# Kernel optimization log

Measured on AMD Instinct MI355X. Metric: run time of the kernel, lower is better.

The kernel has to match this reference:

```python
import jax, jax.numpy as jnp
import numpy as np

N, D, H, O = 2048, 128, 256, 1  # batch, input_dim, hidden_dim, output_dim
LN_EPS = 1e-5


def setup_inputs() -> dict:
    key = jax.random.key(0)
    ks = jax.random.split(key, 10)
    s = lambda fan_in: 1.0 / np.sqrt(fan_in)
    return {
        "array": jax.random.normal(ks[0], (N, D), dtype=jnp.float32),
        # per-feature Linear(1, H) stacked: weight [D, H], bias [D, H]
        "W_in": jax.random.uniform(ks[1], (D, H), jnp.float32, -1.0, 1.0),
        "b_in": jax.random.uniform(ks[2], (D, H), jnp.float32, -1.0, 1.0),
        # FactorAttentionLayer (width D): W: Linear(D, D), V: Linear(D, 1), LayerNorm(D)
        "Wf": jax.random.uniform(ks[3], (D, D), jnp.float32, -s(D), s(D)),
        "bf": jax.random.uniform(ks[4], (D,), jnp.float32, -s(D), s(D)),
        "Vf": jax.random.uniform(ks[5], (D,), jnp.float32, -s(D), s(D)),
        "bv": jnp.zeros((), jnp.float32),
        "ln_g": jnp.ones((D,), jnp.float32),
        "ln_b": jnp.zeros((D,), jnp.float32),
        # fc_hidden: Linear(D*H, H); fc_output: Linear(H, O)  (stored as [in, out])
        "Wh": jax.random.uniform(ks[6], (D * H, H), jnp.float32, -s(D * H), s(D * H)),
        "bh": jax.random.uniform(ks[7], (H,), jnp.float32, -s(D * H), s(D * H)),
        "Wo": jax.random.uniform(ks[8], (H, O), jnp.float32, -s(H), s(H)),
        "bo": jax.random.uniform(ks[9], (O,), jnp.float32, -s(H), s(H)),
    }


def reference(array, W_in, b_in, Wf, bf, Vf, bv, ln_g, ln_b, Wh, bh, Wo, bo):
    # Fused per-feature Linear(1,H)+ReLU: [n, D, H]
    p = jax.nn.relu(array[:, :, None] * W_in[None] + b_in[None])
    # permute(0, 2, 1) -> [n, H, D]
    x = jnp.transpose(p, (0, 2, 1))
    # FactorAttention: tanh-linear, softmax over axis 1 (the H axis), residual mul, LayerNorm over D
    u = jnp.tanh(jnp.einsum('nhd,de->nhe', x, Wf) + bf)          # [n, H, D]
    scores = jnp.einsum('nhd,d->nh', u, Vf) + bv                  # [n, H]
    attn = jax.nn.softmax(scores, axis=1)[:, :, None]             # [n, H, 1]
    y = x + x * attn                                              # [n, H, D]
    mu = jnp.mean(y, axis=-1, keepdims=True)
    var = jnp.mean((y - mu) ** 2, axis=-1, keepdims=True)
    y = (y - mu) * jax.lax.rsqrt(var + LN_EPS) * ln_g + ln_b
    # flatten [n, H*D] and MLP head (dropout = identity in eval)
    xx = y.reshape(y.shape[0], -1)
    h = jax.nn.relu(xx @ Wh + bh)
    return h @ Wo + bo
```

## Files before the change

kernel.cpp:

```cpp
#include <hip/hip_runtime.h>

#define NB 2048
#define DD 128
#define HH 256
#define KF 32768
#define LN_EPS 1e-5f
#define KSPLIT 32
#define KSL (KF / KSPLIT)

typedef __attribute__((ext_vector_type(8))) short short8;
typedef __attribute__((ext_vector_type(4))) float float4_t;
typedef __attribute__((ext_vector_type(4))) float f4;

__device__ __forceinline__ unsigned short f2bf(float f) {
    unsigned int u = __builtin_bit_cast(unsigned int, f);
    u += 0x7fffu + ((u >> 16) & 1u);
    return (unsigned short)(u >> 16);
}

__device__ __forceinline__ unsigned int pkbf(float lo, float hi) {
    unsigned int r;
    asm("v_cvt_pk_bf16_f32 %0, %1, %2" : "=v"(r) : "v"(lo), "v"(hi));
    return r;
}

__device__ __forceinline__ void gl2lds16(const void* g, void* l) {
    __builtin_amdgcn_global_load_lds(
        (const __attribute__((address_space(1))) unsigned int*)g,
        (__attribute__((address_space(3))) unsigned int*)l, 16, 0, 0);
}

__global__ void prep_all(const float* __restrict__ arr, const float* __restrict__ Win,
                         const float* __restrict__ bin, const float* __restrict__ Wh,
                         const float* __restrict__ g, const float* __restrict__ beta,
                         float2* __restrict__ stats, float* __restrict__ WinT,
                         float* __restrict__ binT, unsigned short* __restrict__ WhbT,
                         float* __restrict__ bias2) {
    __shared__ float a_s[4][128];
    __shared__ float tile32[32][33];
    __shared__ unsigned short tile64[64][65];
    __shared__ float red[4][64];
    int bid = blockIdx.x;
    int t = threadIdx.x;

    if (bid >= 576) {
        int pid = bid - 576;
        int kb = pid >> 2;
        int jb = pid & 3;
        int c = t & 63, r4 = t >> 6;
        int k0 = kb * 64;
        float bsum = 0.f;
        for (int rr = r4; rr < 64; rr += 4) {
            int k = k0 + rr, d = k & 127;
            float v = Wh[(long)k * 256 + jb * 64 + c];
            tile64[rr][c] = f2bf(g[d] * v);
            bsum = fmaf(beta[d], v, bsum);
        }
        __syncthreads();
        for (int rr = r4; rr < 64; rr += 4)
            WhbT[(long)(jb * 64 + rr) * KF + k0 + c] = tile64[c][rr];
        red[r4][c] = bsum;
        __syncthreads();
        if (r4 == 0)
            atomicAdd(&bias2[jb * 64 + c],
                      red[0][c] + red[1][c] + red[2][c] + red[3][c]);
        return;
    }
    if (bid >= 512) {
        int tid = bid - 512;
        int mat = tid >> 5;
        int dt = (tid >> 3) & 3;
        int ht = tid & 7;
        const float* src = mat ? bin : Win;
        float* dst = mat ? binT : WinT;
        int c = t & 31, r = t >> 5;
#pragma unroll
        for (int rr = r; rr < 32; rr += 8)
            tile32[rr][c] = src[(dt * 32 + rr) * 256 + ht * 32 + c];
        __syncthreads();
#pragma unroll
        for (int rr = r; rr < 32; rr += 8)
            dst[(ht * 32 + rr) * 128 + dt * 32 + c] = tile32[c][rr];
        return;
    }
    int n0 = bid * 4;
    for (int i = t; i < 512; i += 256) a_s[i >> 7][i & 127] = arr[n0 * 128 + i];
    __syncthreads();
    int h = t;
    float sum[4] = {0.f, 0.f, 0.f, 0.f}, ssq[4] = {0.f, 0.f, 0.f, 0.f};
    for (int d = 0; d < 128; ++d) {
        float w = Win[d * 256 + h];
        float bb = bin[d * 256 + h];
#pragma unroll
        for (int q = 0; q < 4; ++q) {
            float x = fmaxf(fmaf(a_s[q][d], w, bb), 0.f);
            sum[q] += x;
            ssq[q] = fmaf(x, x, ssq[q]);
        }
    }
#pragma unroll
    for (int q = 0; q < 4; ++q) {
        float mu = sum[q] * (1.f / 128.f);
        float var = fmaxf(ssq[q] * (1.f / 128.f) - mu * mu, 0.f);
        float rs = rsqrtf(var + LN_EPS);
        stats[(long)(n0 + q) * HH + h] = make_float2(rs, mu * rs);
    }
}

__global__ __launch_bounds__(512, 4) void gemm_f(
        const float* __restrict__ arr, const float* __restrict__ WinT,
        const float* __restrict__ binT, const float2* __restrict__ stats,
        const unsigned short* __restrict__ Bt,
        float* __restrict__ Cp) {
    __shared__ unsigned short Bs[2][256 * 32];
    __shared__ float Ws[8 * 128];
    __shared__ float Vs[8 * 128];
    __shared__ float2 Ss[128 * 9];
    int bid = blockIdx.x;
    int xcd = bid & 7;
    int idx = bid >> 3;
    int ks = xcd * 4 + (idx >> 4);
    int mt = idx & 15;
    int m0 = mt * 128;
    long k0 = (long)ks * KSL;
    int h0 = ks * 8;
    int t = threadIdx.x;
    int lane = t & 63, wave = t >> 6;
    int wm = (wave >> 1) * 32;
    int wn = (wave & 1) * 128;
    int fr = lane & 15;
    int kch = lane >> 4;
    int fk8 = kch * 8;

    float4_t acc[2][8] = {};

    const unsigned short* Bab = Bt + k0;
    int j0 = t >> 2, sl0 = t & 3;
    long boff0 = (long)j0 * KF + (long)((sl0 ^ ((j0 >> 1) & 3)) << 3);
    long boff1 = boff0 + 128l * KF;

    if (t < 256) {
        *(f4*)&Ws[t * 4] = *(const f4*)(WinT + h0 * 128 + t * 4);
    } else {
        *(f4*)&Vs[(t - 256) * 4] = *(const f4*)(binT + h0 * 128 + (t - 256) * 4);
    }
    {
        int sr = t >> 2, sc = (t & 3) * 2;
        const float2* sp = stats + (long)(m0 + sr) * HH + h0 + sc;
        float2 v0 = sp[0], v1 = sp[1];
        Ss[sr * 9 + sc] = v0;
        Ss[sr * 9 + sc + 1] = v1;
    }
    gl2lds16(Bab + boff0, &Bs[0][t * 8]);
    gl2lds16(Bab + boff1, &Bs[0][(t + 512) * 8]);

    int row0 = m0 + wm + fr;
    f4 aa[2][2];
    __syncthreads();

    for (int it = 0; it < 32; ++it) {
        int q = it >> 3, hl = it & 7, cur = it & 1;
        if (it < 31) {
            int itn = it + 1;
            long kap = (itn & 7) * 128 + (itn >> 3) * 32;
            gl2lds16(Bab + kap + boff0, &Bs[cur ^ 1][t * 8]);
            gl2lds16(Bab + kap + boff1, &Bs[cur ^ 1][(t + 512) * 8]);
        }
        if (hl == 0) {
#pragma unroll
            for (int mi = 0; mi < 2; ++mi) {
                const float* ap = arr + (long)(row0 + mi * 16) * DD + q * 32 + fk8;
                aa[mi][0] = *(const f4*)ap;
                aa[mi][1] = *(const f4*)(ap + 4);
            }
        }
        int wb = hl * 128 + q * 32 + fk8;
        f4 w0 = *(const f4*)&Ws[wb], w1 = *(const f4*)&Ws[wb + 4];
        f4 v0 = *(const f4*)&Vs[wb], v1 = *(const f4*)&Vs[wb + 4];
        short8 af[2];
#pragma unroll
        for (int mi = 0; mi < 2; ++mi) {
            float2 sv = Ss[(wm + mi * 16 + fr) * 9 + hl];
            float rs = sv.x, nm = -sv.y;
            float z0 = fmaf(fmaxf(fmaf(aa[mi][0][0], w0[0], v0[0]), 0.f), rs, nm);
            float z1 = fmaf(fmaxf(fmaf(aa[mi][0][1], w0[1], v0[1]), 0.f), rs, nm);
            float z2 = fmaf(fmaxf(fmaf(aa[mi][0][2], w0[2], v0[2]), 0.f), rs, nm);
            float z3 = fmaf(fmaxf(fmaf(aa[mi][0][3], w0[3], v0[3]), 0.f), rs, nm);
            float z4 = fmaf(fmaxf(fmaf(aa[mi][1][0], w1[0], v1[0]), 0.f), rs, nm);
            float z5 = fmaf(fmaxf(fmaf(aa[mi][1][1], w1[1], v1[1]), 0.f), rs, nm);
            float z6 = fmaf(fmaxf(fmaf(aa[mi][1][2], w1[2], v1[2]), 0.f), rs, nm);
            float z7 = fmaf(fmaxf(fmaf(aa[mi][1][3], w1[3], v1[3]), 0.f), rs, nm);
            union { short8 s; unsigned int u[4]; } pk;
            pk.u[0] = pkbf(z0, z1);
            pk.u[1] = pkbf(z2, z3);
            pk.u[2] = pkbf(z4, z5);
            pk.u[3] = pkbf(z6, z7);
            af[mi] = pk.s;
        }
#pragma unroll
        for (int half = 0; half < 2; ++half) {
            short8 bfv[4];
#pragma unroll
            for (int n4 = 0; n4 < 4; ++n4) {
                int j = wn + (half * 4 + n4) * 16 + fr;
                bfv[n4] = *(const short8*)&Bs[cur][j * 32 + ((kch ^ ((j >> 1) & 3)) << 3)];
            }
#pragma unroll
            for (int mi = 0; mi < 2; ++mi)
#pragma unroll
                for (int n4 = 0; n4 < 4; ++n4)
                    acc[mi][half * 4 + n4] = __builtin_amdgcn_mfma_f32_16x16x32_bf16(
                        af[mi], bfv[n4], acc[mi][half * 4 + n4], 0, 0, 0);
        }
        if (it < 31) __syncthreads();
    }

    int rb = (lane >> 4) * 4;
    float* Cb = Cp + (long)ks * NB * 256;
#pragma unroll
    for (int mi = 0; mi < 2; ++mi) {
#pragma unroll
        for (int ni = 0; ni < 8; ++ni) {
            int n = wn + ni * 16 + fr;
#pragma unroll
            for (int r = 0; r < 4; ++r) {
                int m = m0 + wm + mi * 16 + rb + r;
                Cb[(long)m * 256 + n] = acc[mi][ni][r];
            }
        }
    }
}

__global__ void finale(const float* __restrict__ Cp, const float* __restrict__ bh,
                       const float* __restrict__ Wo, const float* __restrict__ bo,
                       const float* __restrict__ bias2, float* __restrict__ out) {
    __shared__ float red[4];
    int n = blockIdx.x, t = threadIdx.x;
    int lane = t & 63, wave = t >> 6;
    float s = bh[t] + bias2[t];
    for (int sl = 0; sl < KSPLIT; ++sl)
        s += Cp[(long)sl * NB * 256 + (long)n * 256 + t];
    float v = fmaxf(s, 0.f) * Wo[t];
#pragma unroll
    for (int o = 32; o; o >>= 1) v += __shfl_down(v, o);
    if (lane == 0) red[wave] = v;
    __syncthreads();
    if (t == 0) out[n] = red[0] + red[1] + red[2] + red[3] + bo[0];
}

extern "C" void kernel_launch(void* const* d_in, const int* in_sizes, int n_in,
                              void* d_out, int out_size, void* d_ws, size_t ws_size,
                              hipStream_t stream) {
    const float* arr  = (const float*)d_in[0];
    const float* Win  = (const float*)d_in[1];
    const float* bin  = (const float*)d_in[2];
    const float* ln_g = (const float*)d_in[7];
    const float* ln_b = (const float*)d_in[8];
    const float* Wh   = (const float*)d_in[9];
    const float* bh   = (const float*)d_in[10];
    const float* Wo   = (const float*)d_in[11];
    const float* bo   = (const float*)d_in[12];
    float* out = (float*)d_out;

    char* ws = (char*)d_ws;
    unsigned short* WhbT = (unsigned short*)ws;
    float2* stats = (float2*)(ws + 16777216ull);
    float* Cp     = (float*)(ws + 20971520ull);
    float* WinT   = (float*)(ws + 88080384ull);
    float* binT   = (float*)(ws + 88211456ull);
    float* bias2  = (float*)(ws + 88342528ull);

    hipMemsetAsync(bias2, 0, 1024, stream);
    hipLaunchKernelGGL(prep_all, dim3(2624), dim3(256), 0, stream,
                       arr, Win, bin, Wh, ln_g, ln_b, stats, WinT, binT, WhbT, bias2);
    hipLaunchKernelGGL(gemm_f, dim3(512), dim3(512), 0, stream,
                       arr, WinT, binT, stats, WhbT, Cp);
    hipLaunchKernelGGL(finale, dim3(NB), dim3(256), 0, stream,
                       Cp, bh, Wo, bo, bias2, out);
}
```

Measured before the change: 179.6 us.

## Triple-buffer B tiles with prefetch distance two and drop bias atomics

The GEMM's LDS staging for B goes from double to triple buffering. Loads are issued two iterations ahead and guarded by explicit vmcnt waits and raw barriers instead of __syncthreads, so global-to-LDS latency is hidden better. The bias atomicAdd and its memset are replaced by per-block partial sums, which the first four GEMM blocks reduce before starting their main work. The cost is more LDS per block, which may cut occupancy, plus some extra serial work in four blocks.

```diff
diff --git a/kernel.cpp b/kernel.cpp
--- a/kernel.cpp
+++ b/kernel.cpp
@@ -35,7 +35,7 @@
                          const float* __restrict__ g, const float* __restrict__ beta,
                          float2* __restrict__ stats, float* __restrict__ WinT,
                          float* __restrict__ binT, unsigned short* __restrict__ WhbT,
-                         float* __restrict__ bias2) {
+                         float* __restrict__ bias_part) {
     __shared__ float a_s[4][128];
     __shared__ float tile32[32][33];
     __shared__ unsigned short tile64[64][65];
@@ -62,8 +62,7 @@
         red[r4][c] = bsum;
         __syncthreads();
         if (r4 == 0)
-            atomicAdd(&bias2[jb * 64 + c],
-                      red[0][c] + red[1][c] + red[2][c] + red[3][c]);
+            bias_part[pid * 64 + c] = red[0][c] + red[1][c] + red[2][c] + red[3][c];
         return;
     }
     if (bid >= 512) {
@@ -111,12 +110,31 @@
         const float* __restrict__ arr, const float* __restrict__ WinT,
         const float* __restrict__ binT, const float2* __restrict__ stats,
         const unsigned short* __restrict__ Bt,
-        float* __restrict__ Cp) {
-    __shared__ unsigned short Bs[2][256 * 32];
+        float* __restrict__ Cp, const float* __restrict__ bias_part,
+        float* __restrict__ bias2) {
+    __shared__ unsigned short Bs[3][256 * 32];
     __shared__ float Ws[8 * 128];
     __shared__ float Vs[8 * 128];
     __shared__ float2 Ss[128 * 9];
     int bid = blockIdx.x;
+    int t = threadIdx.x;
+
+    if (bid < 4) {
+        int c = t & 63, seg = t >> 6;
+        float s = 0.f;
+        for (int kb = seg * 64; kb < seg * 64 + 64; ++kb)
+            s += bias_part[(kb * 4 + bid) * 64 + c];
+        Ws[seg * 64 + c] = s;
+        __syncthreads();
+        if (seg == 0) {
+            float tot = 0.f;
+#pragma unroll
+            for (int k = 0; k < 8; ++k) tot += Ws[k * 64 + c];
+            bias2[bid * 64 + c] = tot;
+        }
+        __syncthreads();
+    }
+
     int xcd = bid & 7;
     int idx = bid >> 3;
     int ks = xcd * 4 + (idx >> 4);
@@ -124,7 +142,6 @@
     int m0 = mt * 128;
     long k0 = (long)ks * KSL;
     int h0 = ks * 8;
-    int t = threadIdx.x;
     int lane = t & 63, wave = t >> 6;
     int wm = (wave >> 1) * 32;
     int wn = (wave & 1) * 128;
@@ -153,19 +170,18 @@
     }
     gl2lds16(Bab + boff0, &Bs[0][t * 8]);
     gl2lds16(Bab + boff1, &Bs[0][(t + 512) * 8]);
+    gl2lds16(Bab + 128 + boff0, &Bs[1][t * 8]);
+    gl2lds16(Bab + 128 + boff1, &Bs[1][(t + 512) * 8]);
 
     int row0 = m0 + wm + fr;
     f4 aa[2][2];
-    __syncthreads();
-
+    asm volatile("s_waitcnt vmcnt(2) lgkmcnt(0)" ::: "memory");
+    __builtin_amdgcn_s_barrier();
+    __builtin_amdgcn_sched_barrier(0);
+
+    int cur = 0;
     for (int it = 0; it < 32; ++it) {
-        int q = it >> 3, hl = it & 7, cur = it & 1;
-        if (it < 31) {
-            int itn = it + 1;
-            long kap = (itn & 7) * 128 + (itn >> 3) * 32;
-            gl2lds16(Bab + kap + boff0, &Bs[cur ^ 1][t * 8]);
-            gl2lds16(Bab + kap + boff1, &Bs[cur ^ 1][(t + 512) * 8]);
-        }
+        int q = it >> 3, hl = it & 7;
         if (hl == 0) {
 #pragma unroll
             for (int mi = 0; mi < 2; ++mi) {
@@ -173,6 +189,13 @@
                 aa[mi][0] = *(const f4*)ap;
                 aa[mi][1] = *(const f4*)(ap + 4);
             }
+        }
+        if (it < 30) {
+            int itn = it + 2;
+            int nb = cur + 2; if (nb >= 3) nb -= 3;
+            long kap = (itn & 7) * 128 + (itn >> 3) * 32;
+            gl2lds16(Bab + kap + boff0, &Bs[nb][t * 8]);
+            gl2lds16(Bab + kap + boff1, &Bs[nb][(t + 512) * 8]);
         }
         int wb = hl * 128 + q * 32 + fk8;
         f4 w0 = *(const f4*)&Ws[wb], w1 = *(const f4*)&Ws[wb + 4];
@@ -212,7 +235,16 @@
                     acc[mi][half * 4 + n4] = __builtin_amdgcn_mfma_f32_16x16x32_bf16(
                         af[mi], bfv[n4], acc[mi][half * 4 + n4], 0, 0, 0);
         }
-        if (it < 31) __syncthreads();
+        if (it < 30) {
+            asm volatile("s_waitcnt vmcnt(2)" ::: "memory");
+            __builtin_amdgcn_s_barrier();
+            __builtin_amdgcn_sched_barrier(0);
+        } else if (it == 30) {
+            asm volatile("s_waitcnt vmcnt(0)" ::: "memory");
+            __builtin_amdgcn_s_barrier();
+            __builtin_amdgcn_sched_barrier(0);
+        }
+        cur = (cur == 2) ? 0 : cur + 1;
     }
 
     int rb = (lane >> 4) * 4;
@@ -265,16 +297,17 @@
     char* ws = (char*)d_ws;
     unsigned short* WhbT = (unsigned short*)ws;
     float2* stats = (float2*)(ws + 16777216ull);
-    float* Cp     = (float*)(ws + 20971520ull);
-    float* WinT   = (float*)(ws + 88080384ull);
-    float* binT   = (float*)(ws + 88211456ull);
-    float* bias2  = (float*)(ws + 88342528ull);
-
-    hipMemsetAsync(bias2, 0, 1024, stream);
+    float* Cp        = (float*)(ws + 20971520ull);
+    float* WinT      = (float*)(ws + 88080384ull);
+    float* binT      = (float*)(ws + 88211456ull);
+    float* bias2     = (float*)(ws + 88342528ull);
+    float* bias_part = (float*)(ws + 88343552ull);
+
     hipLaunchKernelGGL(prep_all, dim3(2624), dim3(256), 0, stream,
-                       arr, Win, bin, Wh, ln_g, ln_b, stats, WinT, binT, WhbT, bias2);
+                       arr, Win, bin, Wh, ln_g, ln_b, stats, WinT, binT, WhbT,
+                       bias_part);
     hipLaunchKernelGGL(gemm_f, dim3(512), dim3(512), 0, stream,
-                       arr, WinT, binT, stats, WhbT, Cp);
+                       arr, WinT, binT, stats, WhbT, Cp, bias_part, bias2);
     hipLaunchKernelGGL(finale, dim3(NB), dim3(256), 0, stream,
                        Cp, bh, Wo, bo, bias2, out);
 }
```

Measured after the change: 181.9 us. Within noise of the previous version (+1.3%).
